# Kernel tuning notes

Hardware: AMD Instinct MI355X
Metric: run time of the kernel (lower is better)

## Reference

```python
import jax, jax.numpy as jnp
import numpy as np

B, L, D = 1, 2048, 4096
H, KV, HD = 32, 8, 128
ROT = 64  # head_dim * partial_rotary_factor
SCALE = HD ** -0.5
NEG = -1e9


def _apply_rope(x, cos, sin):
    # x: [B, h, L, HD]; rotate only the first ROT dims (partial rotary, rotate-half convention)
    xr, xp = x[..., :ROT], x[..., ROT:]
    x1, x2 = jnp.split(xr, 2, axis=-1)
    rotated = jnp.concatenate([-x2, x1], axis=-1)
    xr = xr * cos[None, None] + rotated * sin[None, None]
    return jnp.concatenate([xr, xp], axis=-1)


def setup_inputs() -> dict:
    key = jax.random.key(0)
    k1, k2, k3 = jax.random.split(key, 3)
    x = jax.random.normal(k1, (B, L, D), jnp.float32)
    w_qkv = jax.random.normal(k2, (D, H * HD + 2 * KV * HD), jnp.float32) * 0.02
    w_o = jax.random.normal(k3, (H * HD, D), jnp.float32) * 0.02
    # causal additive mask, broadcast over batch and heads
    causal = jnp.tril(jnp.ones((L, L), dtype=bool))
    attention_mask = jnp.where(causal, 0.0, NEG).astype(jnp.float32)[None, None]
    # rotary tables over the ROT rotary dims
    inv_freq = 1.0 / (10000.0 ** (jnp.arange(0, ROT, 2, dtype=jnp.float32) / ROT))
    t = jnp.arange(L, dtype=jnp.float32)
    freqs = jnp.outer(t, inv_freq)            # [L, ROT/2]
    emb = jnp.concatenate([freqs, freqs], -1)  # [L, ROT]
    cos, sin = jnp.cos(emb), jnp.sin(emb)
    return {"x": x, "attention_mask": attention_mask, "cos": cos, "sin": sin,
            "w_qkv": w_qkv, "w_o": w_o}


def reference(x, attention_mask, cos, sin, w_qkv, w_o):
    Bx, Lx, _ = x.shape
    qkv = x @ w_qkv                                   # [B, L, H*HD + 2*KV*HD]
    q_pos = H * HD
    kv_pos = q_pos + KV * HD
    q = qkv[:, :, :q_pos].reshape(Bx, Lx, H, HD).transpose(0, 2, 1, 3)
    k = qkv[:, :, q_pos:kv_pos].reshape(Bx, Lx, KV, HD).transpose(0, 2, 1, 3)
    v = qkv[:, :, kv_pos:].reshape(Bx, Lx, KV, HD).transpose(0, 2, 1, 3)
    q = _apply_rope(q, cos, sin)
    k = _apply_rope(k, cos, sin)
    # GQA: duplicate KV heads (as in the original module)
    n_rep = H // KV
    k = jnp.repeat(k, n_rep, axis=1)
    v = jnp.repeat(v, n_rep, axis=1)
    w = jnp.einsum("bhqd,bhkd->bhqk", q, k) * SCALE   # [B, H, L, L]
    w = jax.nn.softmax(w + attention_mask, axis=-1)
    o = jnp.einsum("bhqk,bhkd->bhqd", w, v)           # [B, H, L, HD]
    o = o.transpose(0, 2, 1, 3).reshape(Bx, Lx, H * HD)
    return o @ w_o
```

## Files before the change

### kernel.cpp

```cpp
#include <hip/hip_runtime.h>
#include <stdint.h>

typedef float f32x4 __attribute__((ext_vector_type(4)));
typedef short s16x8 __attribute__((ext_vector_type(8)));
typedef unsigned short u16x4 __attribute__((ext_vector_type(4)));
typedef unsigned short u16x8 __attribute__((ext_vector_type(8)));

#define SCALE_F 0.08838834764831845f

__device__ __forceinline__ unsigned short f32_to_bf16(float f) {
    union { float f; unsigned int u; } v; v.f = f;
    return (unsigned short)((v.u + 0x7FFFu + ((v.u >> 16) & 1u)) >> 16);
}
__device__ __forceinline__ float bf16_to_f32(unsigned short h) {
    union { unsigned int u; float f; } v; v.u = (unsigned int)h << 16;
    return v.f;
}

__device__ __forceinline__ void gload16(const void* g, void* l) {
    __builtin_amdgcn_global_load_lds((const __attribute__((address_space(1))) unsigned int*)g,
                                     (__attribute__((address_space(3))) unsigned int*)l,
                                     16, 0, 0);
}

__global__ void k_conv_bf16(const float* __restrict__ in, unsigned short* __restrict__ out, int n4) {
    int i = blockIdx.x * 256 + threadIdx.x;
    if (i >= n4) return;
    f32x4 v = ((const f32x4*)in)[i];
    u16x4 o;
    o[0] = f32_to_bf16(v[0]); o[1] = f32_to_bf16(v[1]);
    o[2] = f32_to_bf16(v[2]); o[3] = f32_to_bf16(v[3]);
    ((u16x4*)out)[i] = o;
}

__global__ void k_transpose_f32(const float* __restrict__ in, unsigned short* __restrict__ out,
                                int R, int in_ld, int in_off) {
    __shared__ float tile[64][65];
    const int rb = blockIdx.y * 64, cb = blockIdx.x * 64;
    const int t = threadIdx.x;
    const int lr = t >> 4, lc4 = (t & 15) * 4;
#pragma unroll
    for (int i = 0; i < 4; ++i) {
        int r = i * 16 + lr;
        f32x4 v = *(const f32x4*)(in + (size_t)(rb + r) * in_ld + in_off + cb + lc4);
        tile[r][lc4 + 0] = v[0]; tile[r][lc4 + 1] = v[1];
        tile[r][lc4 + 2] = v[2]; tile[r][lc4 + 3] = v[3];
    }
    __syncthreads();
#pragma unroll
    for (int i = 0; i < 4; ++i) {
        int oc = cb + i * 16 + lr;
        u16x4 o;
#pragma unroll
        for (int j = 0; j < 4; ++j)
            o[j] = f32_to_bf16(tile[lc4 + j][i * 16 + lr]);
        *(u16x4*)(out + (size_t)oc * R + rb + lc4) = o;
    }
}

__global__ void k_transpose_b16(const unsigned short* __restrict__ in, unsigned short* __restrict__ out,
                                int R, int in_ld, int in_off) {
    __shared__ unsigned short tile[64][68];
    const int rb = blockIdx.y * 64, cb = blockIdx.x * 64;
    const int t = threadIdx.x;
    const int lr = t >> 4, lc4 = (t & 15) * 4;
#pragma unroll
    for (int i = 0; i < 4; ++i) {
        int r = i * 16 + lr;
        u16x4 v = *(const u16x4*)(in + (size_t)(rb + r) * in_ld + in_off + cb + lc4);
        tile[r][lc4 + 0] = v[0]; tile[r][lc4 + 1] = v[1];
        tile[r][lc4 + 2] = v[2]; tile[r][lc4 + 3] = v[3];
    }
    __syncthreads();
#pragma unroll
    for (int i = 0; i < 4; ++i) {
        int oc = cb + i * 16 + lr;
        u16x4 o;
#pragma unroll
        for (int j = 0; j < 4; ++j)
            o[j] = tile[lc4 + j][i * 16 + lr];
        *(u16x4*)(out + (size_t)oc * R + rb + lc4) = o;
    }
}

template<int BN, typename OUT>
__global__ __launch_bounds__(512, 1)
void k_gemm8p(const unsigned short* __restrict__ A, const unsigned short* __restrict__ Bt,
              OUT* __restrict__ C, int N, int K) {
    __shared__ __align__(16) unsigned short As[2][2][8192];
    __shared__ __align__(16) unsigned short Bs[2][2][8192];
    const int tid = threadIdx.x;
    const int lane = tid & 63, wid = tid >> 6;
    const int g = lane >> 4, l15 = lane & 15;
    const int wm = wid >> 2, wn = wid & 3;
    const int nwg = gridDim.x, bid = blockIdx.x;
    const int swz = (bid & 7) * (nwg >> 3) + (bid >> 3);
    const int ntn = N / BN;
    const int bm = swz / ntn, bn = swz - bm * ntn;
    const int brow = bm << 8, bcol = bn * BN;

    const int rS = tid >> 2;
    const int kcS = (tid & 3) ^ (rS & 3) ^ ((rS >> 2) & 3);
    const unsigned short* sA = A + (size_t)(brow + rS) * K + kcS * 8;
    const unsigned short* sB = Bt + (size_t)(bcol + rS) * K + kcS * 8;
    const int fsw = (g ^ (l15 & 3) ^ ((l15 >> 2) & 3)) * 8;

    f32x4 acc[8][4] = {};
    const int nt = K >> 6;

    auto stA = [&](int t, int kh) {
        unsigned short* d = &As[t & 1][kh][tid * 8];
        const unsigned short* s = sA + (size_t)t * 64 + kh * 32;
        gload16(s, d);
        gload16(s + (size_t)128 * K, d + 4096);
    };
    auto stB = [&](int t, int kh) {
        unsigned short* d = &Bs[t & 1][kh][tid * 8];
        const unsigned short* s = sB + (size_t)t * 64 + kh * 32;
        gload16(s, d);
        gload16(s + (size_t)128 * K, d + 4096);
    };

    stA(0, 0); stB(0, 0); stA(0, 1); stB(0, 1);

    for (int t = 0; t < nt; ++t) {
        const int c = t & 1;
        s16x8 af[4], bf[4];
        if (t + 1 < nt) { stA(t + 1, 0); asm volatile("s_waitcnt vmcnt(6)" ::: "memory"); }
        else            { asm volatile("s_waitcnt vmcnt(4)" ::: "memory"); }
        __builtin_amdgcn_s_barrier();
#pragma unroll
        for (int f = 0; f < 4; ++f)
            af[f] = *(const s16x8*)(&As[c][0][(wm * 128 + f * 16 + l15) * 32 + fsw]);
#pragma unroll
        for (int j = 0; j < 4; ++j)
            bf[j] = *(const s16x8*)(&Bs[c][0][(wn * 64 + j * 16 + l15) * 32 + fsw]);
        __builtin_amdgcn_s_setprio(1);
#pragma unroll
        for (int f = 0; f < 4; ++f)
#pragma unroll
            for (int j = 0; j < 4; ++j)
                acc[f][j] = __builtin_amdgcn_mfma_f32_16x16x32_bf16(af[f], bf[j], acc[f][j], 0, 0, 0);
        __builtin_amdgcn_s_setprio(0);
        if (t + 1 < nt) stB(t + 1, 0);
#pragma unroll
        for (int f = 0; f < 4; ++f)
            af[f] = *(const s16x8*)(&As[c][0][(wm * 128 + 64 + f * 16 + l15) * 32 + fsw]);
        __builtin_amdgcn_s_setprio(1);
#pragma unroll
        for (int f = 0; f < 4; ++f)
#pragma unroll
            for (int j = 0; j < 4; ++j)
                acc[4 + f][j] = __builtin_amdgcn_mfma_f32_16x16x32_bf16(af[f], bf[j], acc[4 + f][j], 0, 0, 0);
        __builtin_amdgcn_s_setprio(0);
        if (t + 1 < nt) { stA(t + 1, 1); asm volatile("s_waitcnt vmcnt(4)" ::: "memory"); }
        else            { asm volatile("s_waitcnt vmcnt(0)" ::: "memory"); }
        __builtin_amdgcn_s_barrier();
#pragma unroll
        for (int f = 0; f < 4; ++f)
            af[f] = *(const s16x8*)(&As[c][1][(wm * 128 + f * 16 + l15) * 32 + fsw]);
#pragma unroll
        for (int j = 0; j < 4; ++j)
            bf[j] = *(const s16x8*)(&Bs[c][1][(wn * 64 + j * 16 + l15) * 32 + fsw]);
        __builtin_amdgcn_s_setprio(1);
#pragma unroll
        for (int f = 0; f < 4; ++f)
#pragma unroll
            for (int j = 0; j < 4; ++j)
                acc[f][j] = __builtin_amdgcn_mfma_f32_16x16x32_bf16(af[f], bf[j], acc[f][j], 0, 0, 0);
        __builtin_amdgcn_s_setprio(0);
        if (t + 1 < nt) stB(t + 1, 1);
#pragma unroll
        for (int f = 0; f < 4; ++f)
            af[f] = *(const s16x8*)(&As[c][1][(wm * 128 + 64 + f * 16 + l15) * 32 + fsw]);
        __builtin_amdgcn_s_setprio(1);
#pragma unroll
        for (int f = 0; f < 4; ++f)
#pragma unroll
            for (int j = 0; j < 4; ++j)
                acc[4 + f][j] = __builtin_amdgcn_mfma_f32_16x16x32_bf16(af[f], bf[j], acc[4 + f][j], 0, 0, 0);
        __builtin_amdgcn_s_setprio(0);
    }

#pragma unroll
    for (int f = 0; f < 8; ++f)
#pragma unroll
        for (int j = 0; j < 4; ++j)
#pragma unroll
            for (int r = 0; r < 4; ++r) {
                const size_t idx = (size_t)(brow + wm * 128 + f * 16 + g * 4 + r) * N
                                   + bcol + wn * 64 + j * 16 + l15;
                if constexpr (sizeof(OUT) == 4) C[idx] = acc[f][j][r];
                else                            C[idx] = f32_to_bf16(acc[f][j][r]);
            }
}

__global__ __launch_bounds__(512, 1)
void k_gemmB(const unsigned short* __restrict__ A, const unsigned short* __restrict__ Bt,
             float* __restrict__ C, int N, int K) {
    __shared__ __align__(16) unsigned short As[2][2][4096];
    __shared__ __align__(16) unsigned short Bs[2][2][8192];
    const int tid = threadIdx.x;
    const int lane = tid & 63, wid = tid >> 6;
    const int g = lane >> 4, l15 = lane & 15;
    const int wm = wid >> 2, wn = wid & 3;
    const int nwg = gridDim.x, bid = blockIdx.x;
    const int swz = (bid & 7) * (nwg >> 3) + (bid >> 3);
    const int ntn = N >> 8;
    const int bm = swz / ntn, bn = swz - bm * ntn;
    const int brow = bm << 7, bcol = bn << 8;

    const int rS = tid >> 2;
    const int kcS = (tid & 3) ^ (rS & 3) ^ ((rS >> 2) & 3);
    const unsigned short* sA = A + (size_t)(brow + rS) * K + kcS * 8;
    const unsigned short* sB = Bt + (size_t)(bcol + rS) * K + kcS * 8;
    const int fsw = (g ^ (l15 & 3) ^ ((l15 >> 2) & 3)) * 8;

    f32x4 acc[4][4] = {};
    const int nt = K >> 6;

    auto stA = [&](int t, int kh) {
        unsigned short* d = &As[t & 1][kh][tid * 8];
        const unsigned short* s = sA + (size_t)t * 64 + kh * 32;
        gload16(s, d);
    };
    auto stB = [&](int t, int kh) {
        unsigned short* d = &Bs[t & 1][kh][tid * 8];
        const unsigned short* s = sB + (size_t)t * 64 + kh * 32;
        gload16(s, d);
        gload16(s + (size_t)128 * K, d + 4096);
    };

    stA(0, 0); stB(0, 0); stA(0, 1); stB(0, 1);

    for (int t = 0; t < nt; ++t) {
        const int c = t & 1;
#pragma unroll
        for (int kh = 0; kh < 2; ++kh) {
            if (t + 1 < nt) { stA(t + 1, kh); stB(t + 1, kh); asm volatile("s_waitcnt vmcnt(6)" ::: "memory"); }
            else if (kh == 0) { asm volatile("s_waitcnt vmcnt(3)" ::: "memory"); }
            else              { asm volatile("s_waitcnt vmcnt(0)" ::: "memory"); }
            __builtin_amdgcn_s_barrier();
            s16x8 af[4], bf[4];
#pragma unroll
            for (int f = 0; f < 4; ++f)
                af[f] = *(const s16x8*)(&As[c][kh][(wm * 64 + f * 16 + l15) * 32 + fsw]);
#pragma unroll
            for (int j = 0; j < 4; ++j)
                bf[j] = *(const s16x8*)(&Bs[c][kh][(wn * 64 + j * 16 + l15) * 32 + fsw]);
            __builtin_amdgcn_s_setprio(1);
#pragma unroll
            for (int f = 0; f < 4; ++f)
#pragma unroll
                for (int j = 0; j < 4; ++j)
                    acc[f][j] = __builtin_amdgcn_mfma_f32_16x16x32_bf16(af[f], bf[j], acc[f][j], 0, 0, 0);
            __builtin_amdgcn_s_setprio(0);
        }
    }

#pragma unroll
    for (int f = 0; f < 4; ++f)
#pragma unroll
        for (int j = 0; j < 4; ++j)
#pragma unroll
            for (int r = 0; r < 4; ++r)
                C[(size_t)(brow + wm * 64 + f * 16 + g * 4 + r) * N
                  + bcol + wn * 64 + j * 16 + l15] = acc[f][j][r];
}

__global__ void k_rope_pack(const unsigned short* __restrict__ qkv, const float* __restrict__ cosT,
                            const float* __restrict__ sinT, unsigned short* __restrict__ Qb,
                            unsigned short* __restrict__ Kb) {
    const int oct = blockIdx.x * 128 + threadIdx.x;
    if (oct >= 640) return;
    const int col = oct * 8;
    const int t = blockIdx.y;
    const int d = col & 127;
    const bool isQ = (col < 4096);
    const float post = isQ ? SCALE_F : 1.0f;
    u16x8 v8 = *(const u16x8*)(qkv + (size_t)t * 6144 + col);
    u16x8 o8;
    if (d < 64) {
        u16x8 p8 = *(const u16x8*)(qkv + (size_t)t * 6144 + (col ^ 32));
        f32x4 c0 = *(const f32x4*)(cosT + t * 64 + d);
        f32x4 c1 = *(const f32x4*)(cosT + t * 64 + d + 4);
        f32x4 s0 = *(const f32x4*)(sinT + t * 64 + d);
        f32x4 s1 = *(const f32x4*)(sinT + t * 64 + d + 4);
        const float sgn = (d < 32) ? -1.f : 1.f;
#pragma unroll
        for (int j = 0; j < 8; ++j) {
            float cc = (j < 4) ? c0[j] : c1[j - 4];
            float ss = (j < 4) ? s0[j] : s1[j - 4];
            float o = (bf16_to_f32(v8[j]) * cc + sgn * bf16_to_f32(p8[j]) * ss) * post;
            o8[j] = f32_to_bf16(o);
        }
    } else {
#pragma unroll
        for (int j = 0; j < 8; ++j)
            o8[j] = f32_to_bf16(bf16_to_f32(v8[j]) * post);
    }
    if (isQ) {
        const int h = col >> 7;
        *(u16x8*)(Qb + ((size_t)h * 2048 + t) * 128 + d) = o8;
    } else {
        const int hk = (col - 4096) >> 7;
        *(u16x8*)(Kb + ((size_t)hk * 2048 + t) * 128 + d) = o8;
    }
}

__global__ __launch_bounds__(256, 2)
void k_attn(const unsigned short* __restrict__ Qb, const unsigned short* __restrict__ Kb,
            const unsigned short* __restrict__ Vt, unsigned short* __restrict__ Ob) {
    __shared__ __align__(16) unsigned short Ks[2][8192];
    __shared__ __align__(16) unsigned short Vs[2][8192];
    __shared__ __align__(16) unsigned short Pl[2][4][1024];
    const int h = blockIdx.y, hk = h >> 2;
    const int qbA = blockIdx.x, qbB = 31 - qbA;
    const int tid = threadIdx.x, lane = tid & 63, wid = tid >> 6;
    const int g = lane >> 4, l15 = lane & 15;
    const int qrA = qbA * 64 + wid * 16, qrB = qbB * 64 + wid * 16;
    const int swz = (l15 & 7) << 4;

    s16x8 aqA[4], aqB[4];
#pragma unroll
    for (int kc = 0; kc < 4; ++kc) {
        aqA[kc] = *(const s16x8*)(Qb + ((size_t)h * 2048 + qrA + l15) * 128 + kc * 32 + g * 8);
        aqB[kc] = *(const s16x8*)(Qb + ((size_t)h * 2048 + qrB + l15) * 128 + kc * 32 + g * 8);
    }

    const unsigned short* gK = Kb + ((size_t)hk * 2048 + (tid & 63)) * 128 + (tid >> 6) * 8;
    const unsigned short* gV = Vt + ((size_t)hk * 128 + (tid & 127)) * 2048 + (tid >> 7) * 8;

    auto stage = [&](int kb) {
        unsigned short* dK = Ks[kb & 1] + tid * 8;
        unsigned short* dV = Vs[kb & 1] + tid * 8;
        const unsigned short* sK = gK + (size_t)kb * 8192;
        const unsigned short* sV = gV + kb * 64;
#pragma unroll
        for (int i = 0; i < 4; ++i) gload16(sK + i * 32, dK + i * 2048);
#pragma unroll
        for (int i = 0; i < 4; ++i) gload16(sV + i * 16, dV + i * 2048);
    };

    f32x4 oaccA[8] = {}, oaccB[8] = {};
    float mA = -1e30f, lA = 0.f, mB = -1e30f, lB = 0.f;

    auto qk = [&](const s16x8* aq, f32x4* s, const unsigned short* ks) {
        __builtin_amdgcn_s_setprio(1);
#pragma unroll
        for (int kc = 0; kc < 4; ++kc)
#pragma unroll
            for (int kt = 0; kt < 4; ++kt) {
                s16x8 kf = *(const s16x8*)(ks + ((kc * 4 + g) * 64 + kt * 16 + l15) * 8);
                s[kt] = __builtin_amdgcn_mfma_f32_16x16x32_bf16(kf, aq[kc], s[kt], 0, 0, 0);
            }
        __builtin_amdgcn_s_setprio(0);
    };

    auto sm = [&](f32x4* s, f32x4* oacc, float& mr, float& lr, int qrow0, int kb, char* pw) {
        const int q = qrow0 + l15;
        if (kb * 64 + 63 > qrow0) {
#pragma unroll
            for (int kt = 0; kt < 4; ++kt)
#pragma unroll
                for (int r = 0; r < 4; ++r)
                    if (kb * 64 + kt * 16 + g * 4 + r > q) s[kt][r] = -3e38f;
        }
        float mx = -3e38f;
#pragma unroll
        for (int kt = 0; kt < 4; ++kt)
#pragma unroll
            for (int r = 0; r < 4; ++r) mx = fmaxf(mx, s[kt][r]);
        mx = fmaxf(mx, __shfl_xor(mx, 16));
        mx = fmaxf(mx, __shfl_xor(mx, 32));
        if (!__all(mx - mr <= 8.0f)) {
            const float mnew = fmaxf(mr, mx);
            const float scal = __expf(mr - mnew);
            mr = mnew;
            float so[4];
#pragma unroll
            for (int r = 0; r < 4; ++r) so[r] = __shfl(scal, g * 4 + r, 16);
#pragma unroll
            for (int j = 0; j < 8; ++j) {
                oacc[j][0] *= so[0]; oacc[j][1] *= so[1];
                oacc[j][2] *= so[2]; oacc[j][3] *= so[3];
            }
            lr *= scal;
        }
        float ps = 0.f;
#pragma unroll
        for (int kt = 0; kt < 4; ++kt)
#pragma unroll
            for (int r = 0; r < 4; ++r) {
                float p = __expf(s[kt][r] - mr);
                s[kt][r] = p;
                ps += p;
            }
        ps += __shfl_xor(ps, 16);
        ps += __shfl_xor(ps, 32);
        lr += ps;
#pragma unroll
        for (int kt = 0; kt < 4; ++kt) {
            unsigned int w0 = (unsigned int)f32_to_bf16(s[kt][0]) | ((unsigned int)f32_to_bf16(s[kt][1]) << 16);
            unsigned int w1 = (unsigned int)f32_to_bf16(s[kt][2]) | ((unsigned int)f32_to_bf16(s[kt][3]) << 16);
            const int b0 = (l15 * 128 + kt * 32 + g * 8) ^ swz;
            *(unsigned int*)(pw + b0) = w0;
            *(unsigned int*)(pw + b0 + 4) = w1;
        }
    };

    auto pv = [&](f32x4* oacc, char* pw, const unsigned short* vs) {
        __builtin_amdgcn_s_setprio(1);
#pragma unroll
        for (int kc = 0; kc < 2; ++kc) {
            s16x8 pa = *(const s16x8*)(pw + ((l15 * 128 + kc * 64 + g * 16) ^ swz));
#pragma unroll
            for (int j = 0; j < 8; ++j) {
                s16x8 bv = *(const s16x8*)(vs + ((kc * 4 + g) * 128 + j * 16 + l15) * 8);
                oacc[j] = __builtin_amdgcn_mfma_f32_16x16x32_bf16(pa, bv, oacc[j], 0, 0, 0);
            }
        }
        __builtin_amdgcn_s_setprio(0);
    };

    const int nkb = qbB + 1;
    stage(0);
    for (int kb = 0; kb < nkb; ++kb) {
        if (kb + 1 < nkb) {
            stage(kb + 1);
            asm volatile("s_waitcnt vmcnt(8)" ::: "memory");
        } else {
            asm volatile("s_waitcnt vmcnt(0)" ::: "memory");
        }
        __builtin_amdgcn_s_barrier();
        const unsigned short* ks = Ks[kb & 1];
        const unsigned short* vs = Vs[kb & 1];
        const bool doA = (kb <= qbA);
        f32x4 sB_[4] = {}, sA_[4] = {};
        qk(aqB, sB_, ks);
        if (doA) qk(aqA, sA_, ks);
        sm(sB_, oaccB, mB, lB, qrB, kb, (char*)Pl[1][wid]);
        pv(oaccB, (char*)Pl[1][wid], vs);
        if (doA) {
            sm(sA_, oaccA, mA, lA, qrA, kb, (char*)Pl[0][wid]);
            pv(oaccA, (char*)Pl[0][wid], vs);
        }
        __builtin_amdgcn_s_barrier();
    }
    float liA[4], liB[4];
#pragma unroll
    for (int r = 0; r < 4; ++r) {
        liA[r] = 1.f / __shfl(lA, g * 4 + r, 16);
        liB[r] = 1.f / __shfl(lB, g * 4 + r, 16);
    }
#pragma unroll
    for (int j = 0; j < 8; ++j)
#pragma unroll
        for (int r = 0; r < 4; ++r) {
            Ob[(size_t)(qrA + g * 4 + r) * 4096 + h * 128 + j * 16 + l15] = f32_to_bf16(oaccA[j][r] * liA[r]);
            Ob[(size_t)(qrB + g * 4 + r) * 4096 + h * 128 + j * 16 + l15] = f32_to_bf16(oaccB[j][r] * liB[r]);
        }
}

extern "C" void kernel_launch(void* const* d_in, const int* in_sizes, int n_in,
                              void* d_out, int out_size, void* d_ws, size_t ws_size,
                              hipStream_t stream) {
    const float* x     = (const float*)d_in[0];
    const float* cosT  = (const float*)d_in[2];
    const float* sinT  = (const float*)d_in[3];
    const float* w_qkv = (const float*)d_in[4];
    const float* w_o   = (const float*)d_in[5];
    float* out = (float*)d_out;

    char* ws = (char*)d_ws;
    unsigned short* wT   = (unsigned short*)(ws + 0);
    unsigned short* qkvb = (unsigned short*)(ws + 50331648);
    unsigned short* Ob   = (unsigned short*)(ws + 50331648);
    unsigned short* xb   = (unsigned short*)(ws + 100663296);
    unsigned short* Qb   = xb;
    unsigned short* Kb   = (unsigned short*)(ws + 117440512);
    unsigned short* Vt   = (unsigned short*)(ws + 121634816);

    k_conv_bf16<<<8192, 256, 0, stream>>>(x, xb, 2097152);
    k_transpose_f32<<<dim3(96, 64), 256, 0, stream>>>(w_qkv, wT, 4096, 6144, 0);
    k_gemm8p<256, unsigned short><<<192, 512, 0, stream>>>(xb, wT, qkvb, 6144, 4096);
    k_rope_pack<<<dim3(5, 2048), 128, 0, stream>>>(qkvb, cosT, sinT, Qb, Kb);
    k_transpose_b16<<<dim3(16, 32), 256, 0, stream>>>(qkvb, Vt, 2048, 6144, 5120);
    k_transpose_f32<<<dim3(64, 64), 256, 0, stream>>>(w_o, wT, 4096, 4096, 0);
    k_attn<<<dim3(16, 32), 256, 0, stream>>>(Qb, Kb, Vt, Ob);
    k_gemmB<<<256, 512, 0, stream>>>(Ob, wT, out, 4096, 4096);
}
```

Measured before the change: 361.8 us.

## Retile QKV GEMM to 128x384 for full CU coverage and interleave attention MFMAs

Replaces the 256x256-tile QKV projection GEMM (192 workgroups) with a 128x384 tile variant launched on 256 workgroups, so all compute units get one tile. Its pipeline becomes a simpler per-k-half loop that issues the A and B loads together. In the attention kernel, the QK and PV MFMAs for the two query blocks are interleaved so each K/V fragment loaded from LDS feeds two MFMAs, and the softmax steps are grouped between them. The trade-off is a lower arithmetic intensity per tile in the GEMM and higher register pressure in attention.

```diff
diff --git a/kernel.cpp b/kernel.cpp
--- a/kernel.cpp
+++ b/kernel.cpp
@@ -83,21 +83,20 @@
     }
 }
 
-template<int BN, typename OUT>
 __global__ __launch_bounds__(512, 1)
-void k_gemm8p(const unsigned short* __restrict__ A, const unsigned short* __restrict__ Bt,
-              OUT* __restrict__ C, int N, int K) {
-    __shared__ __align__(16) unsigned short As[2][2][8192];
-    __shared__ __align__(16) unsigned short Bs[2][2][8192];
+void k_gemmA(const unsigned short* __restrict__ A, const unsigned short* __restrict__ Bt,
+             unsigned short* __restrict__ C, int N, int K) {
+    __shared__ __align__(16) unsigned short As[2][2][4096];
+    __shared__ __align__(16) unsigned short Bs[2][2][12288];
     const int tid = threadIdx.x;
     const int lane = tid & 63, wid = tid >> 6;
     const int g = lane >> 4, l15 = lane & 15;
     const int wm = wid >> 2, wn = wid & 3;
     const int nwg = gridDim.x, bid = blockIdx.x;
     const int swz = (bid & 7) * (nwg >> 3) + (bid >> 3);
-    const int ntn = N / BN;
+    const int ntn = N / 384;
     const int bm = swz / ntn, bn = swz - bm * ntn;
-    const int brow = bm << 8, bcol = bn * BN;
+    const int brow = bm << 7, bcol = bn * 384;
 
     const int rS = tid >> 2;
     const int kcS = (tid & 3) ^ (rS & 3) ^ ((rS >> 2) & 3);
@@ -105,94 +104,56 @@
     const unsigned short* sB = Bt + (size_t)(bcol + rS) * K + kcS * 8;
     const int fsw = (g ^ (l15 & 3) ^ ((l15 >> 2) & 3)) * 8;
 
-    f32x4 acc[8][4] = {};
+    f32x4 acc[4][6] = {};
     const int nt = K >> 6;
 
     auto stA = [&](int t, int kh) {
         unsigned short* d = &As[t & 1][kh][tid * 8];
-        const unsigned short* s = sA + (size_t)t * 64 + kh * 32;
-        gload16(s, d);
-        gload16(s + (size_t)128 * K, d + 4096);
+        gload16(sA + (size_t)t * 64 + kh * 32, d);
     };
     auto stB = [&](int t, int kh) {
         unsigned short* d = &Bs[t & 1][kh][tid * 8];
         const unsigned short* s = sB + (size_t)t * 64 + kh * 32;
         gload16(s, d);
         gload16(s + (size_t)128 * K, d + 4096);
+        gload16(s + (size_t)256 * K, d + 8192);
     };
 
     stA(0, 0); stB(0, 0); stA(0, 1); stB(0, 1);
 
     for (int t = 0; t < nt; ++t) {
         const int c = t & 1;
-        s16x8 af[4], bf[4];
-        if (t + 1 < nt) { stA(t + 1, 0); asm volatile("s_waitcnt vmcnt(6)" ::: "memory"); }
-        else            { asm volatile("s_waitcnt vmcnt(4)" ::: "memory"); }
-        __builtin_amdgcn_s_barrier();
-#pragma unroll
-        for (int f = 0; f < 4; ++f)
-            af[f] = *(const s16x8*)(&As[c][0][(wm * 128 + f * 16 + l15) * 32 + fsw]);
-#pragma unroll
-        for (int j = 0; j < 4; ++j)
-            bf[j] = *(const s16x8*)(&Bs[c][0][(wn * 64 + j * 16 + l15) * 32 + fsw]);
-        __builtin_amdgcn_s_setprio(1);
-#pragma unroll
-        for (int f = 0; f < 4; ++f)
-#pragma unroll
-            for (int j = 0; j < 4; ++j)
-                acc[f][j] = __builtin_amdgcn_mfma_f32_16x16x32_bf16(af[f], bf[j], acc[f][j], 0, 0, 0);
-        __builtin_amdgcn_s_setprio(0);
-        if (t + 1 < nt) stB(t + 1, 0);
-#pragma unroll
-        for (int f = 0; f < 4; ++f)
-            af[f] = *(const s16x8*)(&As[c][0][(wm * 128 + 64 + f * 16 + l15) * 32 + fsw]);
-        __builtin_amdgcn_s_setprio(1);
-#pragma unroll
-        for (int f = 0; f < 4; ++f)
-#pragma unroll
-            for (int j = 0; j < 4; ++j)
-                acc[4 + f][j] = __builtin_amdgcn_mfma_f32_16x16x32_bf16(af[f], bf[j], acc[4 + f][j], 0, 0, 0);
-        __builtin_amdgcn_s_setprio(0);
-        if (t + 1 < nt) { stA(t + 1, 1); asm volatile("s_waitcnt vmcnt(4)" ::: "memory"); }
-        else            { asm volatile("s_waitcnt vmcnt(0)" ::: "memory"); }
-        __builtin_amdgcn_s_barrier();
-#pragma unroll
-        for (int f = 0; f < 4; ++f)
-            af[f] = *(const s16x8*)(&As[c][1][(wm * 128 + f * 16 + l15) * 32 + fsw]);
-#pragma unroll
-        for (int j = 0; j < 4; ++j)
-            bf[j] = *(const s16x8*)(&Bs[c][1][(wn * 64 + j * 16 + l15) * 32 + fsw]);
-        __builtin_amdgcn_s_setprio(1);
-#pragma unroll
-        for (int f = 0; f < 4; ++f)
-#pragma unroll
-            for (int j = 0; j < 4; ++j)
-                acc[f][j] = __builtin_amdgcn_mfma_f32_16x16x32_bf16(af[f], bf[j], acc[f][j], 0, 0, 0);
-        __builtin_amdgcn_s_setprio(0);
-        if (t + 1 < nt) stB(t + 1, 1);
-#pragma unroll
-        for (int f = 0; f < 4; ++f)
-            af[f] = *(const s16x8*)(&As[c][1][(wm * 128 + 64 + f * 16 + l15) * 32 + fsw]);
-        __builtin_amdgcn_s_setprio(1);
-#pragma unroll
-        for (int f = 0; f < 4; ++f)
-#pragma unroll
-            for (int j = 0; j < 4; ++j)
-                acc[4 + f][j] = __builtin_amdgcn_mfma_f32_16x16x32_bf16(af[f], bf[j], acc[4 + f][j], 0, 0, 0);
-        __builtin_amdgcn_s_setprio(0);
-    }
-
-#pragma unroll
-    for (int f = 0; f < 8; ++f)
-#pragma unroll
-        for (int j = 0; j < 4; ++j)
-#pragma unroll
-            for (int r = 0; r < 4; ++r) {
-                const size_t idx = (size_t)(brow + wm * 128 + f * 16 + g * 4 + r) * N
-                                   + bcol + wn * 64 + j * 16 + l15;
-                if constexpr (sizeof(OUT) == 4) C[idx] = acc[f][j][r];
-                else                            C[idx] = f32_to_bf16(acc[f][j][r]);
-            }
+#pragma unroll
+        for (int kh = 0; kh < 2; ++kh) {
+            if (t + 1 < nt)   { stA(t + 1, kh); stB(t + 1, kh); asm volatile("s_waitcnt vmcnt(8)" ::: "memory"); }
+            else if (kh == 0) { asm volatile("s_waitcnt vmcnt(4)" ::: "memory"); }
+            else              { asm volatile("s_waitcnt vmcnt(0)" ::: "memory"); }
+            __builtin_amdgcn_s_barrier();
+            s16x8 af[4], bf[6];
+#pragma unroll
+            for (int f = 0; f < 4; ++f)
+                af[f] = *(const s16x8*)(&As[c][kh][(wm * 64 + f * 16 + l15) * 32 + fsw]);
+#pragma unroll
+            for (int j = 0; j < 6; ++j)
+                bf[j] = *(const s16x8*)(&Bs[c][kh][(wn * 96 + j * 16 + l15) * 32 + fsw]);
+            __builtin_amdgcn_s_setprio(1);
+#pragma unroll
+            for (int f = 0; f < 4; ++f)
+#pragma unroll
+                for (int j = 0; j < 6; ++j)
+                    acc[f][j] = __builtin_amdgcn_mfma_f32_16x16x32_bf16(af[f], bf[j], acc[f][j], 0, 0, 0);
+            __builtin_amdgcn_s_setprio(0);
+        }
+    }
+
+#pragma unroll
+    for (int f = 0; f < 4; ++f)
+#pragma unroll
+        for (int j = 0; j < 6; ++j)
+#pragma unroll
+            for (int r = 0; r < 4; ++r)
+                C[(size_t)(brow + wm * 64 + f * 16 + g * 4 + r) * N
+                  + bcol + wn * 96 + j * 16 + l15] = f32_to_bf16(acc[f][j][r]);
 }
 
 __global__ __launch_bounds__(512, 1)
@@ -220,9 +181,7 @@
     const int nt = K >> 6;
 
     auto stA = [&](int t, int kh) {
-        unsigned short* d = &As[t & 1][kh][tid * 8];
-        const unsigned short* s = sA + (size_t)t * 64 + kh * 32;
-        gload16(s, d);
+        gload16(sA + (size_t)t * 64 + kh * 32, &As[t & 1][kh][tid * 8]);
     };
     auto stB = [&](int t, int kh) {
         unsigned short* d = &Bs[t & 1][kh][tid * 8];
@@ -345,18 +304,6 @@
     f32x4 oaccA[8] = {}, oaccB[8] = {};
     float mA = -1e30f, lA = 0.f, mB = -1e30f, lB = 0.f;
 
-    auto qk = [&](const s16x8* aq, f32x4* s, const unsigned short* ks) {
-        __builtin_amdgcn_s_setprio(1);
-#pragma unroll
-        for (int kc = 0; kc < 4; ++kc)
-#pragma unroll
-            for (int kt = 0; kt < 4; ++kt) {
-                s16x8 kf = *(const s16x8*)(ks + ((kc * 4 + g) * 64 + kt * 16 + l15) * 8);
-                s[kt] = __builtin_amdgcn_mfma_f32_16x16x32_bf16(kf, aq[kc], s[kt], 0, 0, 0);
-            }
-        __builtin_amdgcn_s_setprio(0);
-    };
-
     auto sm = [&](f32x4* s, f32x4* oacc, float& mr, float& lr, int qrow0, int kb, char* pw) {
         const int q = qrow0 + l15;
         if (kb * 64 + 63 > qrow0) {
@@ -409,20 +356,6 @@
         }
     };
 
-    auto pv = [&](f32x4* oacc, char* pw, const unsigned short* vs) {
-        __builtin_amdgcn_s_setprio(1);
-#pragma unroll
-        for (int kc = 0; kc < 2; ++kc) {
-            s16x8 pa = *(const s16x8*)(pw + ((l15 * 128 + kc * 64 + g * 16) ^ swz));
-#pragma unroll
-            for (int j = 0; j < 8; ++j) {
-                s16x8 bv = *(const s16x8*)(vs + ((kc * 4 + g) * 128 + j * 16 + l15) * 8);
-                oacc[j] = __builtin_amdgcn_mfma_f32_16x16x32_bf16(pa, bv, oacc[j], 0, 0, 0);
-            }
-        }
-        __builtin_amdgcn_s_setprio(0);
-    };
-
     const int nkb = qbB + 1;
     stage(0);
     for (int kb = 0; kb < nkb; ++kb) {
@@ -435,16 +368,57 @@
         __builtin_amdgcn_s_barrier();
         const unsigned short* ks = Ks[kb & 1];
         const unsigned short* vs = Vs[kb & 1];
+        char* pwA = (char*)Pl[0][wid];
+        char* pwB = (char*)Pl[1][wid];
         const bool doA = (kb <= qbA);
         f32x4 sB_[4] = {}, sA_[4] = {};
-        qk(aqB, sB_, ks);
-        if (doA) qk(aqA, sA_, ks);
-        sm(sB_, oaccB, mB, lB, qrB, kb, (char*)Pl[1][wid]);
-        pv(oaccB, (char*)Pl[1][wid], vs);
+        __builtin_amdgcn_s_setprio(1);
         if (doA) {
-            sm(sA_, oaccA, mA, lA, qrA, kb, (char*)Pl[0][wid]);
-            pv(oaccA, (char*)Pl[0][wid], vs);
-        }
+#pragma unroll
+            for (int kc = 0; kc < 4; ++kc)
+#pragma unroll
+                for (int kt = 0; kt < 4; ++kt) {
+                    s16x8 kf = *(const s16x8*)(ks + ((kc * 4 + g) * 64 + kt * 16 + l15) * 8);
+                    sB_[kt] = __builtin_amdgcn_mfma_f32_16x16x32_bf16(kf, aqB[kc], sB_[kt], 0, 0, 0);
+                    sA_[kt] = __builtin_amdgcn_mfma_f32_16x16x32_bf16(kf, aqA[kc], sA_[kt], 0, 0, 0);
+                }
+        } else {
+#pragma unroll
+            for (int kc = 0; kc < 4; ++kc)
+#pragma unroll
+                for (int kt = 0; kt < 4; ++kt) {
+                    s16x8 kf = *(const s16x8*)(ks + ((kc * 4 + g) * 64 + kt * 16 + l15) * 8);
+                    sB_[kt] = __builtin_amdgcn_mfma_f32_16x16x32_bf16(kf, aqB[kc], sB_[kt], 0, 0, 0);
+                }
+        }
+        __builtin_amdgcn_s_setprio(0);
+        sm(sB_, oaccB, mB, lB, qrB, kb, pwB);
+        if (doA) sm(sA_, oaccA, mA, lA, qrA, kb, pwA);
+        __builtin_amdgcn_s_setprio(1);
+        if (doA) {
+#pragma unroll
+            for (int kc = 0; kc < 2; ++kc) {
+                s16x8 paB = *(const s16x8*)(pwB + ((l15 * 128 + kc * 64 + g * 16) ^ swz));
+                s16x8 paA = *(const s16x8*)(pwA + ((l15 * 128 + kc * 64 + g * 16) ^ swz));
+#pragma unroll
+                for (int j = 0; j < 8; ++j) {
+                    s16x8 bv = *(const s16x8*)(vs + ((kc * 4 + g) * 128 + j * 16 + l15) * 8);
+                    oaccB[j] = __builtin_amdgcn_mfma_f32_16x16x32_bf16(paB, bv, oaccB[j], 0, 0, 0);
+                    oaccA[j] = __builtin_amdgcn_mfma_f32_16x16x32_bf16(paA, bv, oaccA[j], 0, 0, 0);
+                }
+            }
+        } else {
+#pragma unroll
+            for (int kc = 0; kc < 2; ++kc) {
+                s16x8 paB = *(const s16x8*)(pwB + ((l15 * 128 + kc * 64 + g * 16) ^ swz));
+#pragma unroll
+                for (int j = 0; j < 8; ++j) {
+                    s16x8 bv = *(const s16x8*)(vs + ((kc * 4 + g) * 128 + j * 16 + l15) * 8);
+                    oaccB[j] = __builtin_amdgcn_mfma_f32_16x16x32_bf16(paB, bv, oaccB[j], 0, 0, 0);
+                }
+            }
+        }
+        __builtin_amdgcn_s_setprio(0);
         __builtin_amdgcn_s_barrier();
     }
     float liA[4], liB[4];
@@ -483,7 +457,7 @@
 
     k_conv_bf16<<<8192, 256, 0, stream>>>(x, xb, 2097152);
     k_transpose_f32<<<dim3(96, 64), 256, 0, stream>>>(w_qkv, wT, 4096, 6144, 0);
-    k_gemm8p<256, unsigned short><<<192, 512, 0, stream>>>(xb, wT, qkvb, 6144, 4096);
+    k_gemmA<<<256, 512, 0, stream>>>(xb, wT, qkvb, 6144, 4096);
     k_rope_pack<<<dim3(5, 2048), 128, 0, stream>>>(qkvb, cosT, sinT, Qb, Kb);
     k_transpose_b16<<<dim3(16, 32), 256, 0, stream>>>(qkvb, Vt, 2048, 6144, 5120);
     k_transpose_f32<<<dim3(64, 64), 256, 0, stream>>>(w_o, wT, 4096, 4096, 0);
```

After: 359.5 us. No clear change (-0.6%).
